# Optimization experiments

Measured on AMD Instinct MI355X. Metric: run time of the kernel, lower is better.

The kernel has to match this reference:

```python
import jax, jax.numpy as jnp
import numpy as np
import math

B, T, D, H, DM = 2, 2048, 1024, 16, 256
DK = D // H

def setup_inputs() -> dict:
    key = jax.random.key(0)
    ks = jax.random.split(key, 13)
    s = 0.02
    return {
        "Hx": jax.random.normal(ks[0], (B, D, T, 1), jnp.float32),
        "Hf": jax.random.normal(ks[1], (B, T, D), jnp.float32),
        "Gm": jax.random.normal(ks[2], (B, T, DM), jnp.float32),
        "Wg": jax.random.normal(ks[3], (T, DM), jnp.float32) * s,
        "bg": jax.random.normal(ks[4], (T,), jnp.float32) * s,
        "Wq": jax.random.normal(ks[5], (D, 2 * D), jnp.float32) * s,
        "bq": jax.random.normal(ks[6], (D,), jnp.float32) * s,
        "Wk": jax.random.normal(ks[7], (D, 2 * D), jnp.float32) * s,
        "bk": jax.random.normal(ks[8], (D,), jnp.float32) * s,
        "Wv": jax.random.normal(ks[9], (D, D), jnp.float32) * s,
        "bv": jax.random.normal(ks[10], (D,), jnp.float32) * s,
        "Wo": jax.random.normal(ks[11], (D, D), jnp.float32) * s,
        "bo": jax.random.normal(ks[12], (D,), jnp.float32) * s,
    }

def reference(Hx, Hf, Gm, Wg, bg, Wq, bq, Wk, bk, Wv, bv, Wo, bo):
    # Hx: (B, D, T, 1) -> (B, T, D)
    hx = jnp.transpose(Hx[..., 0], (0, 2, 1))
    h_cat = jnp.concatenate([hx, Hf], axis=-1)          # (B, T, 2D)
    Q = h_cat @ Wq.T + bq                               # (B, T, D)
    K = h_cat @ Wk.T + bk
    V = hx @ Wv.T + bv
    # split heads: (B, H, T, DK)
    Q = Q.reshape(B, T, H, DK).transpose(0, 2, 1, 3)
    K = K.reshape(B, T, H, DK).transpose(0, 2, 1, 3)
    V = V.reshape(B, T, H, DK).transpose(0, 2, 1, 3)
    scores = jnp.einsum('bhqd,bhkd->bhqk', Q, K) / math.sqrt(DK)
    bias = Gm @ Wg.T + bg                                # (B, T, T)
    scores = scores + bias[:, None, :, :]
    attn = jax.nn.softmax(scores, axis=-1)
    out = jnp.einsum('bhqk,bhkd->bhqd', attn, V)
    out = out.transpose(0, 2, 1, 3).reshape(B, T, D)
    return out @ Wo.T + bo
```

## Files before the change

### kernel.cpp

```cpp
#include <hip/hip_runtime.h>
#include <hip/hip_bf16.h>

using bf16 = __hip_bfloat16;
typedef __attribute__((ext_vector_type(8))) __bf16 bf16x8;
typedef __attribute__((ext_vector_type(4))) float f32x4;

#define GLB_AS(p) ((const __attribute__((address_space(1))) unsigned int*)(p))
#define LDS_AS(p) ((__attribute__((address_space(3))) unsigned int*)(p))

__device__ __forceinline__ void async_copy16(const void* g, void* l) {
  __builtin_amdgcn_global_load_lds(GLB_AS(g), LDS_AS(l), 16, 0, 0);
}

__device__ __forceinline__ f32x4 mfma16x16x32(bf16x8 a, bf16x8 b, f32x4 c) {
  return __builtin_amdgcn_mfma_f32_16x16x32_bf16(a, b, c, 0, 0, 0);
}

__device__ __forceinline__ float bfu2f(unsigned short u) {
  union { unsigned int i; float f; } x;
  x.i = (unsigned int)u << 16;
  return x.f;
}

#define LOG2E 1.44269504f

__global__ __launch_bounds__(256) void pack_hx(const float* __restrict__ Hx,
                                               bf16* __restrict__ hcat) {
  __shared__ float tile[64][65];
  const int t0 = blockIdx.x * 64, d0 = blockIdx.y * 64, b = blockIdx.z;
  const int c = threadIdx.x & 63, r0 = threadIdx.x >> 6;
#pragma unroll
  for (int i = 0; i < 16; ++i) {
    const int rd = r0 + i * 4;
    tile[rd][c] = Hx[((size_t)(b * 1024 + d0 + rd)) * 2048 + t0 + c];
  }
  __syncthreads();
#pragma unroll
  for (int i = 0; i < 16; ++i) {
    const int ct = r0 + i * 4;
    hcat[((size_t)(b * 2048 + t0 + ct)) * 2048 + d0 + c] =
        __float2bfloat16(tile[c][ct]);
  }
}

__global__ __launch_bounds__(256) void pack_all(
    const float* __restrict__ Hf, const float* __restrict__ Wq,
    const float* __restrict__ Wk, const float* __restrict__ Wv,
    const float* __restrict__ Wo, const float* __restrict__ Wg,
    const float* __restrict__ Gm, const float* __restrict__ bq,
    const float* __restrict__ bk, const float* __restrict__ bv,
    bf16* __restrict__ hcat, bf16* __restrict__ Wqkvb, bf16* __restrict__ Wob,
    bf16* __restrict__ Wgb, bf16* __restrict__ Gmb,
    float* __restrict__ qkvbias) {
  const int gid = blockIdx.x * 256 + threadIdx.x;
  const float* src = nullptr;
  bf16* dst = nullptr;
  int lg = 0, ldo = 0, off = 0, idx = 0;
  bool zero = false;
  if (gid < 1048576) { idx = gid; src = Hf; dst = hcat; lg = 8; ldo = 2048; off = 1024; }
  else if (gid < 1572864) { idx = gid - 1048576; src = Wq; dst = Wqkvb; lg = 9; ldo = 2048; }
  else if (gid < 2097152) { idx = gid - 1572864; src = Wk; dst = Wqkvb + (size_t)1024 * 2048; lg = 9; ldo = 2048; }
  else if (gid < 2359296) { idx = gid - 2097152; src = Wv; dst = Wqkvb + (size_t)2048 * 2048; lg = 8; ldo = 2048; }
  else if (gid < 2621440) { idx = gid - 2359296; zero = true; dst = Wqkvb + (size_t)2048 * 2048 + 1024; lg = 8; ldo = 2048; }
  else if (gid < 2883584) { idx = gid - 2621440; src = Wo; dst = Wob; lg = 8; ldo = 1024; }
  else if (gid < 3014656) { idx = gid - 2883584; src = Wg; dst = Wgb; lg = 6; ldo = 256; }
  else if (gid < 3276800) { idx = gid - 3014656; src = Gm; dst = Gmb; lg = 6; ldo = 256; }
  else if (gid < 3277056) { const int i = gid - 3276800; ((float4*)qkvbias)[i] = ((const float4*)bq)[i]; return; }
  else if (gid < 3277312) { const int i = gid - 3277056; ((float4*)(qkvbias + 1024))[i] = ((const float4*)bk)[i]; return; }
  else { const int i = gid - 3277312; ((float4*)(qkvbias + 2048))[i] = ((const float4*)bv)[i]; return; }
  const int row = idx >> lg, c = idx & ((1 << lg) - 1);
  bf16* o = dst + (size_t)row * ldo + off + c * 4;
  __align__(8) bf16 tmp[4];
  if (zero) {
    tmp[0] = tmp[1] = tmp[2] = tmp[3] = __float2bfloat16(0.f);
  } else {
    const float4 v = ((const float4*)src)[(size_t)idx];
    tmp[0] = __float2bfloat16(v.x); tmp[1] = __float2bfloat16(v.y);
    tmp[2] = __float2bfloat16(v.z); tmp[3] = __float2bfloat16(v.w);
  }
  *(ushort4*)o = *(const ushort4*)tmp;
}

__global__ __launch_bounds__(512, 2) void gemm_qkv_bias(
    const bf16* __restrict__ hcat, const bf16* __restrict__ Wqkv,
    const float* __restrict__ qkvbias, const bf16* __restrict__ Gmb,
    const bf16* __restrict__ Wgb, const float* __restrict__ bg,
    bf16* __restrict__ QKb, bf16* __restrict__ Vt, bf16* __restrict__ biasS) {
  __shared__ __align__(16) bf16 AS[2][256][64];
  __shared__ __align__(16) bf16 BS[2][256][64];
  const int lin = blockIdx.x;
  const bool isqkv = lin < 192;
  int m0, n0, Kd, KT, nit2;
  const bf16 *Ag, *Bg;
  const float* biasv;
  if (isqkv) {
    const int xcd = lin & 7, kk = lin >> 3;
    const int mloc = kk / 6, nloc = kk - mloc * 6;
    m0 = ((xcd >> 1) * 4 + mloc) * 256;
    n0 = ((xcd & 1) * 6 + nloc) * 256;
    Ag = hcat; Bg = Wqkv; biasv = qkvbias;
    Kd = 2048; KT = 32; nit2 = 16;
  } else {
    const int l2 = lin - 192;
    m0 = (l2 >> 3) * 256;
    n0 = (l2 & 7) * 256;
    Ag = Gmb; Bg = Wgb; biasv = bg;
    Kd = 256; KT = 4; nit2 = 2;
  }
  const int tid = threadIdx.x, lane = tid & 63, w = tid >> 6;
  const int w8 = w * 8, ln3 = lane >> 3, ch = lane & 7;
  const int fr = lane & 15, ck = lane >> 4;
  const int wm64 = (w >> 2) * 64;
  const int wn32 = (w & 3) * 32;

  f32x4 acc[8][4];
  const f32x4 fzero = {0.f, 0.f, 0.f, 0.f};
#pragma unroll
  for (int i = 0; i < 8; ++i)
#pragma unroll
    for (int j = 0; j < 4; ++j) acc[i][j] = fzero;

  auto stageA = [&](int buf, int mh, int kt) {
    const int k0 = kt * 64;
#pragma unroll
    for (int l = 0; l < 2; ++l) {
      const int rit = mh * 128 + l * 64 + w8 + ln3;
      async_copy16(Ag + (size_t)(m0 + rit) * Kd + k0 + ((ch ^ ln3) << 3),
                   (char*)&AS[buf][0][0] + ((mh * 128 + l * 64 + w8) << 7));
    }
  };
  auto stageB = [&](int buf, int nh, int kt) {
    const int k0 = kt * 64;
#pragma unroll
    for (int l = 0; l < 2; ++l) {
      const int rit = nh * 128 + l * 64 + w8 + ln3;
      async_copy16(Bg + (size_t)(n0 + rit) * Kd + k0 + ((ch ^ ln3) << 3),
                   (char*)&BS[buf][0][0] + ((nh * 128 + l * 64 + w8) << 7));
    }
  };

  bf16x8 af[4][2], bA[2][2], bB[2][2];
  auto ldA = [&](int buf, int mh) {
#pragma unroll
    for (int i = 0; i < 4; ++i)
#pragma unroll
      for (int ks = 0; ks < 2; ++ks)
        af[i][ks] = *(const bf16x8*)(
            &AS[buf][mh * 128 + wm64 + i * 16 + fr][0] +
            (((ks * 4 + ck) ^ (fr & 7)) << 3));
  };
  auto ldB = [&](bf16x8 (&dst)[2][2], int buf, int nh) {
#pragma unroll
    for (int j = 0; j < 2; ++j)
#pragma unroll
      for (int ks = 0; ks < 2; ++ks)
        dst[j][ks] = *(const bf16x8*)(
            &BS[buf][nh * 128 + wn32 + j * 16 + fr][0] +
            (((ks * 4 + ck) ^ (fr & 7)) << 3));
  };

#define BAR() __builtin_amdgcn_s_barrier()
#define LGKM0() asm volatile("s_waitcnt lgkmcnt(0)" ::: "memory")
#define MMAQ(MH, NH, BF)                                                      \
  __builtin_amdgcn_s_setprio(1);                                              \
  _Pragma("unroll") for (int i_ = 0; i_ < 4; ++i_) {                          \
    _Pragma("unroll") for (int j_ = 0; j_ < 2; ++j_) {                        \
      acc[(MH) * 4 + i_][(NH) * 2 + j_] = mfma16x16x32(                       \
          af[i_][0], BF[j_][0], acc[(MH) * 4 + i_][(NH) * 2 + j_]);           \
      acc[(MH) * 4 + i_][(NH) * 2 + j_] = mfma16x16x32(                       \
          af[i_][1], BF[j_][1], acc[(MH) * 4 + i_][(NH) * 2 + j_]);           \
    }                                                                         \
  }                                                                           \
  __builtin_amdgcn_s_setprio(0);

  stageA(0, 0, 0); stageB(0, 0, 0); stageB(0, 1, 0); stageA(0, 1, 0);
  stageA(1, 0, 1); stageB(1, 0, 1);
  asm volatile("s_waitcnt vmcnt(4)" ::: "memory");
  BAR();

  for (int it = 0; it < nit2; ++it) {
    const int kodd = 2 * it + 1;
    const int kn0 = (2 * it + 2 < KT) ? 2 * it + 2 : KT - 1;
    const int kn1 = (2 * it + 3 < KT) ? 2 * it + 3 : KT - 1;

    ldA(0, 0); ldB(bA, 0, 0);
    stageB(1, 1, kodd);
    asm volatile("s_waitcnt lgkmcnt(8)");
    BAR(); LGKM0();
    MMAQ(0, 0, bA);
    BAR();
    ldB(bB, 0, 1);
    stageA(1, 1, kodd);
    BAR(); LGKM0();
    MMAQ(0, 1, bB);
    BAR();
    ldA(0, 1);
    stageA(0, 0, kn0);
    BAR(); LGKM0();
    MMAQ(1, 0, bA);
    BAR();
    stageB(0, 0, kn0);
    asm volatile("s_waitcnt vmcnt(4)" ::: "memory");
    BAR();
    MMAQ(1, 1, bB);
    BAR();
    ldA(1, 0); ldB(bA, 1, 0);
    stageB(0, 1, kn0);
    asm volatile("s_waitcnt lgkmcnt(8)");
    BAR(); LGKM0();
    MMAQ(0, 0, bA);
    BAR();
    ldB(bB, 1, 1);
    stageA(0, 1, kn0);
    BAR(); LGKM0();
    MMAQ(0, 1, bB);
    BAR();
    ldA(1, 1);
    stageA(1, 0, kn1);
    BAR(); LGKM0();
    MMAQ(1, 0, bA);
    BAR();
    stageB(1, 0, kn1);
    asm volatile("s_waitcnt vmcnt(4)" ::: "memory");
    BAR();
    MMAQ(1, 1, bB);
    BAR();
  }
  asm volatile("s_waitcnt vmcnt(0)" ::: "memory");

  const int erow = (lane >> 4) * 4, ecol = lane & 15;
  if (!isqkv) {
#pragma unroll
    for (int ai = 0; ai < 8; ++ai) {
      const int gm0 = m0 + (ai >> 2) * 128 + wm64 + (ai & 3) * 16 + erow;
#pragma unroll
      for (int bj = 0; bj < 4; ++bj) {
        const int gn = n0 + (bj >> 1) * 128 + wn32 + (bj & 1) * 16 + ecol;
        const float bv = biasv[gn];
#pragma unroll
        for (int r = 0; r < 4; ++r)
          biasS[(size_t)(gm0 + r) * 2048 + gn] =
              __float2bfloat16((acc[ai][bj][r] + bv) * LOG2E);
      }
    }
  } else if (n0 < 2048) {
    const float sc = (n0 < 1024) ? 0.125f * LOG2E : 1.0f;
#pragma unroll
    for (int ai = 0; ai < 8; ++ai) {
      const int gm0 = m0 + (ai >> 2) * 128 + wm64 + (ai & 3) * 16 + erow;
#pragma unroll
      for (int bj = 0; bj < 4; ++bj) {
        const int gn = n0 + (bj >> 1) * 128 + wn32 + (bj & 1) * 16 + ecol;
        const float bv = biasv[gn];
#pragma unroll
        for (int r = 0; r < 4; ++r)
          QKb[(size_t)(gm0 + r) * 2048 + gn] =
              __float2bfloat16((acc[ai][bj][r] + bv) * sc);
      }
    }
  } else {
#pragma unroll
    for (int ai = 0; ai < 8; ++ai) {
      const int gm0 = m0 + (ai >> 2) * 128 + wm64 + (ai & 3) * 16 + erow;
      const int bb = gm0 >> 11;
      const int t = gm0 & 2047;
#pragma unroll
      for (int bj = 0; bj < 4; ++bj) {
        const int gn = n0 + (bj >> 1) * 128 + wn32 + (bj & 1) * 16 + ecol;
        const float bv = biasv[gn];
        const int d = gn - 2048;
        __align__(8) bf16 tmp[4];
#pragma unroll
        for (int r = 0; r < 4; ++r)
          tmp[r] = __float2bfloat16(acc[ai][bj][r] + bv);
        *(ushort4*)(Vt + ((size_t)(bb * 1024 + d)) * 2048 + t) =
            *(const ushort4*)tmp;
      }
    }
  }
#undef MMAQ
#undef LGKM0
#undef BAR
}

__global__ __launch_bounds__(256) void gemm_out(const bf16* __restrict__ A,
                                                const bf16* __restrict__ W,
                                                const float* __restrict__ biasv,
                                                float* __restrict__ C) {
  __shared__ __align__(16) bf16 As[2][128 * 64];
  __shared__ __align__(16) bf16 Bs[2][64 * 64];
  const int lin = blockIdx.x;
  const int xcd = lin & 7;
  const int kk = lin >> 3;
  const int m0 = (kk >> 1) * 128;
  const int n0 = (xcd * 2 + (kk & 1)) * 64;
  const int tid = threadIdx.x, lane = tid & 63, w = tid >> 6;
  const int wm = (w >> 1) * 64, wn = (w & 1) * 32;
  const int fr = lane & 15;
  const int ck = lane >> 4;

  f32x4 acc[4][2];
  const f32x4 fzero = {0.f, 0.f, 0.f, 0.f};
#pragma unroll
  for (int i = 0; i < 4; ++i)
#pragma unroll
    for (int j = 0; j < 2; ++j) acc[i][j] = fzero;

  auto stage = [&](int it, int buf) {
    const int k0 = it * 64;
#pragma unroll
    for (int is = 0; is < 4; ++is) {
      const int off = is * 4096 + w * 1024;
      const int row = (off >> 7) + (lane >> 3);
      const int sch = ((lane & 7) ^ (row & 7)) * 8;
      async_copy16(A + (size_t)(m0 + row) * 1024 + k0 + sch,
                   (char*)As[buf] + off);
      if (is < 2)
        async_copy16(W + (size_t)(n0 + row) * 1024 + k0 + sch,
                     (char*)Bs[buf] + off);
    }
  };

  stage(0, 0);
  __syncthreads();
  for (int it = 0; it < 16; ++it) {
    const int cur = it & 1;
    if (it + 1 < 16) stage(it + 1, cur ^ 1);
#pragma unroll
    for (int ks = 0; ks < 2; ++ks) {
      bf16x8 af[4], bfr[2];
      const int swk0 = (((ks * 4 + ck) ^ (fr & 7))) * 8;
#pragma unroll
      for (int i = 0; i < 4; ++i)
        af[i] = *(const bf16x8*)(As[cur] + (wm + i * 16 + fr) * 64 + swk0);
#pragma unroll
      for (int j = 0; j < 2; ++j)
        bfr[j] = *(const bf16x8*)(Bs[cur] + (wn + j * 16 + fr) * 64 + swk0);
#pragma unroll
      for (int i = 0; i < 4; ++i)
#pragma unroll
        for (int j = 0; j < 2; ++j)
          acc[i][j] = mfma16x16x32(af[i], bfr[j], acc[i][j]);
    }
    __syncthreads();
  }
  const int erow = (lane >> 4) * 4;
  const int ecol = lane & 15;
#pragma unroll
  for (int i = 0; i < 4; ++i) {
    const int gm0 = m0 + wm + i * 16 + erow;
#pragma unroll
    for (int j = 0; j < 2; ++j) {
      const int gn = n0 + wn + j * 16 + ecol;
      const float bv = biasv[gn];
#pragma unroll
      for (int r = 0; r < 4; ++r)
        C[(size_t)(gm0 + r) * 1024 + gn] = acc[i][j][r] + bv;
    }
  }
}

__global__ __launch_bounds__(512, 2) void flash_attn(
    const bf16* __restrict__ Qm, const bf16* __restrict__ Km,
    const bf16* __restrict__ Vtm, const bf16* __restrict__ biasS,
    float* __restrict__ Op0, float* __restrict__ Op1,
    float* __restrict__ lpart) {
  __shared__ __align__(16) bf16 Ks[2][2][64 * 64];
  __shared__ __align__(16) bf16 Vs[2][2][64 * 64];
  __shared__ __align__(16) bf16 Ps[8 * 32 * 72];
  const int lin = blockIdx.x;
  const int hp = lin >> 5;
  const int g = lin & 31;
  const int half = g & 1;
  const int b = (g >> 1) & 1;
  const int q0 = (g >> 2) * 256;
  const int tid = threadIdx.x, lane = tid & 63, w = tid >> 6;
  const int ql = lane & 15, qk = lane >> 4;
  const int T = 2048, D = 1024;
  const int sw0 = (qk ^ (ql & 7)) * 8;
  const int sw1 = ((qk + 4) ^ (ql & 7)) * 8;
  const int ln3 = lane >> 3;
  const int sch = ((lane & 7) ^ ln3) << 3;
  const int jb = half * 16;

  bf16x8 qf[2][2][2];
#pragma unroll
  for (int hh = 0; hh < 2; ++hh)
#pragma unroll
    for (int qt = 0; qt < 2; ++qt)
#pragma unroll
      for (int ks = 0; ks < 2; ++ks)
        qf[hh][qt][ks] = *(const bf16x8*)(
            Qm + (size_t)(b * T + q0 + w * 32 + qt * 16 + ql) * 2048 +
            (hp * 2 + hh) * 64 + ks * 32 + qk * 8);

  f32x4 acc[2][4][2];
  const f32x4 fzero = {0.f, 0.f, 0.f, 0.f};
#pragma unroll
  for (int hh = 0; hh < 2; ++hh)
#pragma unroll
    for (int dt = 0; dt < 4; ++dt)
#pragma unroll
      for (int qt = 0; qt < 2; ++qt) acc[hh][dt][qt] = fzero;
  float lp[2][2] = {{0.f, 0.f}, {0.f, 0.f}};

  const bf16* kbase0 = Km + (size_t)(b * T) * 2048 + (hp * 2) * 64;
  const bf16* vbase0 = Vtm + (size_t)(b * D + hp * 2 * 64) * 2048;
  const bf16* bb0 = biasS + (size_t)(b * T + q0 + w * 32 + ql) * 2048 + qk * 4;
  bf16* pb = Ps + w * 2304;
  const int srow = w * 8 + ln3;

  ushort4 bqA[2][4], bqB[2][4];

#define STAGEKV(BUF, JJ)                                                       \
  _Pragma("unroll") for (int hh_ = 0; hh_ < 2; ++hh_) {                        \
    async_copy16(kbase0 + (size_t)((JJ) * 64 + srow) * 2048 + hh_ * 64 + sch,  \
                 (char*)Ks[BUF][hh_] + w * 1024);                              \
    async_copy16(vbase0 + (size_t)(hh_ * 64 + srow) * 2048 + (JJ) * 64 + sch,  \
                 (char*)Vs[BUF][hh_] + w * 1024);                              \
  }

  STAGEKV(0, jb)
#pragma unroll
  for (int qt = 0; qt < 2; ++qt)
#pragma unroll
    for (int jt = 0; jt < 4; ++jt)
      bqA[qt][jt] =
          *(const ushort4*)(bb0 + (size_t)qt * 16 * 2048 + jb * 64 + jt * 16);

#define QKHEAD(HH, CUR, BQC)                                                   \
  {                                                                            \
    const bf16* ksp_ = Ks[CUR][HH];                                            \
    _Pragma("unroll") for (int jt_ = 0; jt_ < 4; ++jt_) {                      \
      const bf16x8 kf0_ = *(const bf16x8*)(ksp_ + (jt_ * 16 + ql) * 64 + sw0); \
      const bf16x8 kf1_ = *(const bf16x8*)(ksp_ + (jt_ * 16 + ql) * 64 + sw1); \
      _Pragma("unroll") for (int qt_ = 0; qt_ < 2; ++qt_) {                    \
        f32x4 c_;                                                              \
        c_[0] = bfu2f(BQC[qt_][jt_].x); c_[1] = bfu2f(BQC[qt_][jt_].y);        \
        c_[2] = bfu2f(BQC[qt_][jt_].z); c_[3] = bfu2f(BQC[qt_][jt_].w);        \
        c_ = mfma16x16x32(kf0_, qf[HH][qt_][0], c_);                           \
        c_ = mfma16x16x32(kf1_, qf[HH][qt_][1], c_);                           \
        __align__(8) bf16 t4_[4];                                              \
        _Pragma("unroll") for (int r_ = 0; r_ < 4; ++r_) {                     \
          const float pv_ = __builtin_amdgcn_exp2f(c_[r_]);                    \
          lp[HH][qt_] += pv_;                                                  \
          t4_[r_] = __float2bfloat16(pv_);                                     \
        }                                                                      \
        *(ushort4*)(pb + (qt_ * 16 + ql) * 72 + jt_ * 16 + qk * 4) =           \
            *(const ushort4*)t4_;                                              \
      }                                                                        \
    }                                                                          \
  }

#define PVHEAD(HH, CUR)                                                        \
  {                                                                            \
    const bf16* vsp_ = Vs[CUR][HH];                                            \
    __builtin_amdgcn_s_setprio(1);                                             \
    _Pragma("unroll") for (int ks_ = 0; ks_ < 2; ++ks_) {                      \
      const bf16x8 pf0_ = *(const bf16x8*)(pb + ql * 72 + ks_ * 32 + qk * 8);  \
      const bf16x8 pf1_ =                                                      \
          *(const bf16x8*)(pb + (16 + ql) * 72 + ks_ * 32 + qk * 8);           \
      const int sw_ = ks_ ? sw1 : sw0;                                         \
      _Pragma("unroll") for (int dt_ = 0; dt_ < 4; ++dt_) {                    \
        const bf16x8 vf_ =                                                     \
            *(const bf16x8*)(vsp_ + (dt_ * 16 + ql) * 64 + sw_);               \
        acc[HH][dt_][0] = mfma16x16x32(pf0_, vf_, acc[HH][dt_][0]);            \
        acc[HH][dt_][1] = mfma16x16x32(pf1_, vf_, acc[HH][dt_][1]);            \
      }                                                                        \
    }                                                                          \
    __builtin_amdgcn_s_setprio(0);                                             \
  }

#define AITER(JV, CUR, BQC, BQN)                                               \
  {                                                                            \
    const int jn_ = (JV) < 15 ? (JV) + 1 : 15;                                 \
    const int jjn_ = jb + jn_;                                                 \
    STAGEKV((CUR) ^ 1, jjn_)                                                   \
    _Pragma("unroll") for (int qt_ = 0; qt_ < 2; ++qt_)                        \
        _Pragma("unroll") for (int jt_ = 0; jt_ < 4; ++jt_)                    \
            BQN[qt_][jt_] = *(const ushort4*)(bb0 + (size_t)qt_ * 16 * 2048 +  \
                                              jjn_ * 64 + jt_ * 16);           \
    asm volatile("s_waitcnt vmcnt(12)" ::: "memory");                          \
    __builtin_amdgcn_s_barrier();                                              \
    QKHEAD(0, CUR, BQC)                                                        \
    PVHEAD(0, CUR)                                                             \
    QKHEAD(1, CUR, BQC)                                                        \
    PVHEAD(1, CUR)                                                             \
    __builtin_amdgcn_s_barrier();                                              \
  }

  for (int jp = 0; jp < 8; ++jp) {
    AITER(jp * 2, 0, bqA, bqB)
    AITER(jp * 2 + 1, 1, bqB, bqA)
  }
#undef AITER
#undef QKHEAD
#undef PVHEAD
#undef STAGEKV
  asm volatile("s_waitcnt vmcnt(0)" ::: "memory");

#pragma unroll
  for (int hh = 0; hh < 2; ++hh)
#pragma unroll
    for (int qt = 0; qt < 2; ++qt) {
      lp[hh][qt] += __shfl_xor(lp[hh][qt], 16);
      lp[hh][qt] += __shfl_xor(lp[hh][qt], 32);
    }
  if (qk == 0) {
#pragma unroll
    for (int hh = 0; hh < 2; ++hh)
#pragma unroll
      for (int qt = 0; qt < 2; ++qt)
        lpart[half * 65536 + (b * 16 + hp * 2 + hh) * 2048 + q0 + w * 32 +
              qt * 16 + ql] = lp[hh][qt];
  }
  float* Op = half ? Op1 : Op0;
#pragma unroll
  for (int hh = 0; hh < 2; ++hh)
#pragma unroll
    for (int qt = 0; qt < 2; ++qt)
#pragma unroll
      for (int r = 0; r < 4; ++r) {
        const size_t orow =
            (size_t)(b * T + q0 + w * 32 + qt * 16 + qk * 4 + r);
#pragma unroll
        for (int dt = 0; dt < 4; ++dt)
          Op[orow * 1024 + (hp * 2 + hh) * 64 + dt * 16 + ql] =
              acc[hh][dt][qt][r];
      }
}

__global__ __launch_bounds__(256) void combine(const float* __restrict__ O0,
                                               const float* __restrict__ O1,
                                               const float* __restrict__ lpart,
                                               bf16* __restrict__ AOut) {
  const int idx = blockIdx.x * 256 + threadIdx.x;
  const int row = idx >> 8;
  const int col = (idx & 255) * 4;
  const int b = row >> 11, q = row & 2047, h = col >> 6;
  const int li = (b * 16 + h) * 2048 + q;
  const float inv = __builtin_amdgcn_rcpf(lpart[li] + lpart[65536 + li]);
  const float4 a = *(const float4*)(O0 + (size_t)row * 1024 + col);
  const float4 c = *(const float4*)(O1 + (size_t)row * 1024 + col);
  __align__(8) bf16 t[4] = {
      __float2bfloat16((a.x + c.x) * inv), __float2bfloat16((a.y + c.y) * inv),
      __float2bfloat16((a.z + c.z) * inv), __float2bfloat16((a.w + c.w) * inv)};
  *(ushort4*)(AOut + (size_t)row * 1024 + col) = *(const ushort4*)t;
}

extern "C" void kernel_launch(void* const* d_in, const int* in_sizes, int n_in,
                              void* d_out, int out_size, void* d_ws,
                              size_t ws_size, hipStream_t stream) {
  (void)in_sizes; (void)n_in; (void)out_size; (void)ws_size;
  const float* Hx = (const float*)d_in[0];
  const float* Hf = (const float*)d_in[1];
  const float* Gm = (const float*)d_in[2];
  const float* Wg = (const float*)d_in[3];
  const float* bg = (const float*)d_in[4];
  const float* Wq = (const float*)d_in[5];
  const float* bq = (const float*)d_in[6];
  const float* Wk = (const float*)d_in[7];
  const float* bk = (const float*)d_in[8];
  const float* Wv = (const float*)d_in[9];
  const float* bv = (const float*)d_in[10];
  const float* Wo = (const float*)d_in[11];
  const float* bo = (const float*)d_in[12];
  float* out = (float*)d_out;

  char* p = (char*)d_ws;
  bf16* hcat = (bf16*)p;   p += (size_t)4096 * 2048 * 2;
  bf16* QKb = (bf16*)p;    p += (size_t)4096 * 2048 * 2;
  bf16* Vtb = (bf16*)p;    p += (size_t)4096 * 1024 * 2;
  bf16* biasS = (bf16*)p;  p += (size_t)4096 * 2048 * 2;
  bf16* AOut = (bf16*)p;   p += (size_t)4096 * 1024 * 2;
  bf16* Wqkvb = (bf16*)p;  p += (size_t)3072 * 2048 * 2;
  bf16* Wob = (bf16*)p;    p += (size_t)1024 * 1024 * 2;
  bf16* Wgb = (bf16*)p;    p += (size_t)2048 * 256 * 2;
  bf16* Gmb = (bf16*)p;    p += (size_t)4096 * 256 * 2;
  float* qkvbias = (float*)p; p += (size_t)3072 * 4;
  float* Op1 = (float*)p;  p += (size_t)4096 * 1024 * 4;
  float* lpart = (float*)p; p += (size_t)2 * 65536 * 4;
  float* Op0 = (float*)hcat;

  pack_hx<<<dim3(32, 16, 2), 256, 0, stream>>>(Hx, hcat);
  pack_all<<<dim3(12803), 256, 0, stream>>>(Hf, Wq, Wk, Wv, Wo, Wg, Gm, bq, bk,
                                            bv, hcat, Wqkvb, Wob, Wgb, Gmb,
                                            qkvbias);
  gemm_qkv_bias<<<dim3(320), 512, 0, stream>>>(hcat, Wqkvb, qkvbias, Gmb,
                                               Wgb, bg, QKb, Vtb, biasS);
  flash_attn<<<dim3(256), 512, 0, stream>>>(QKb, QKb + 1024, Vtb, biasS,
                                            Op0, Op1, lpart);
  combine<<<dim3(4096), 256, 0, stream>>>(Op0, Op1, lpart, AOut);
  gemm_out<<<dim3(512), 256, 0, stream>>>(AOut, Wob, bo, out);
}
```

Before: 280.3 us.

## Split flash attention to one head per block with swizzled unpadded P tile

Each flash_attn block now handles one head instead of a pair, which doubles the grid to 512 blocks and halves the LDS and register footprint so launch bounds can request four blocks per CU. The padded P buffer is replaced by a 64-wide XOR-swizzled layout to avoid bank conflicts without padding. The block-index decode is reordered and the vmcnt wait is adjusted for fewer outstanding copies. In exchange, the bias tile is now read separately for each head, doubling bias traffic, and the work done between barriers is halved.

```diff
diff --git a/kernel.cpp b/kernel.cpp
--- a/kernel.cpp
+++ b/kernel.cpp
@@ -360,20 +360,21 @@
   }
 }
 
-__global__ __launch_bounds__(512, 2) void flash_attn(
+__global__ __launch_bounds__(512, 4) void flash_attn(
     const bf16* __restrict__ Qm, const bf16* __restrict__ Km,
     const bf16* __restrict__ Vtm, const bf16* __restrict__ biasS,
     float* __restrict__ Op0, float* __restrict__ Op1,
     float* __restrict__ lpart) {
-  __shared__ __align__(16) bf16 Ks[2][2][64 * 64];
-  __shared__ __align__(16) bf16 Vs[2][2][64 * 64];
-  __shared__ __align__(16) bf16 Ps[8 * 32 * 72];
+  __shared__ __align__(16) bf16 Ks[2][64 * 64];
+  __shared__ __align__(16) bf16 Vs[2][64 * 64];
+  __shared__ __align__(16) bf16 Ps[8 * 32 * 64];
   const int lin = blockIdx.x;
-  const int hp = lin >> 5;
+  const int h = lin >> 5;
   const int g = lin & 31;
-  const int half = g & 1;
-  const int b = (g >> 1) & 1;
-  const int q0 = (g >> 2) * 256;
+  const int qblk = g >> 2;
+  const int half = (g >> 1) & 1;
+  const int b = g & 1;
+  const int q0 = qblk * 256;
   const int tid = threadIdx.x, lane = tid & 63, w = tid >> 6;
   const int ql = lane & 15, qk = lane >> 4;
   const int T = 2048, D = 1024;
@@ -382,42 +383,39 @@
   const int ln3 = lane >> 3;
   const int sch = ((lane & 7) ^ ln3) << 3;
   const int jb = half * 16;
-
-  bf16x8 qf[2][2][2];
-#pragma unroll
-  for (int hh = 0; hh < 2; ++hh)
-#pragma unroll
-    for (int qt = 0; qt < 2; ++qt)
-#pragma unroll
-      for (int ks = 0; ks < 2; ++ks)
-        qf[hh][qt][ks] = *(const bf16x8*)(
-            Qm + (size_t)(b * T + q0 + w * 32 + qt * 16 + ql) * 2048 +
-            (hp * 2 + hh) * 64 + ks * 32 + qk * 8);
-
-  f32x4 acc[2][4][2];
+  const int qla7 = ql & 7;
+
+  bf16x8 qf[2][2];
+#pragma unroll
+  for (int qt = 0; qt < 2; ++qt)
+#pragma unroll
+    for (int ks = 0; ks < 2; ++ks)
+      qf[qt][ks] = *(const bf16x8*)(
+          Qm + (size_t)(b * T + q0 + w * 32 + qt * 16 + ql) * 2048 + h * 64 +
+          ks * 32 + qk * 8);
+
+  f32x4 acc[4][2];
   const f32x4 fzero = {0.f, 0.f, 0.f, 0.f};
 #pragma unroll
-  for (int hh = 0; hh < 2; ++hh)
-#pragma unroll
-    for (int dt = 0; dt < 4; ++dt)
-#pragma unroll
-      for (int qt = 0; qt < 2; ++qt) acc[hh][dt][qt] = fzero;
-  float lp[2][2] = {{0.f, 0.f}, {0.f, 0.f}};
-
-  const bf16* kbase0 = Km + (size_t)(b * T) * 2048 + (hp * 2) * 64;
-  const bf16* vbase0 = Vtm + (size_t)(b * D + hp * 2 * 64) * 2048;
+  for (int dt = 0; dt < 4; ++dt)
+#pragma unroll
+    for (int qt = 0; qt < 2; ++qt) acc[dt][qt] = fzero;
+  float lp[2] = {0.f, 0.f};
+
+  const bf16* kbase = Km + (size_t)(b * T) * 2048 + h * 64;
+  const bf16* vbase = Vtm + (size_t)(b * D + h * 64) * 2048;
   const bf16* bb0 = biasS + (size_t)(b * T + q0 + w * 32 + ql) * 2048 + qk * 4;
-  bf16* pb = Ps + w * 2304;
+  bf16* pb = Ps + w * 2048;
   const int srow = w * 8 + ln3;
 
   ushort4 bqA[2][4], bqB[2][4];
 
 #define STAGEKV(BUF, JJ)                                                       \
-  _Pragma("unroll") for (int hh_ = 0; hh_ < 2; ++hh_) {                        \
-    async_copy16(kbase0 + (size_t)((JJ) * 64 + srow) * 2048 + hh_ * 64 + sch,  \
-                 (char*)Ks[BUF][hh_] + w * 1024);                              \
-    async_copy16(vbase0 + (size_t)(hh_ * 64 + srow) * 2048 + (JJ) * 64 + sch,  \
-                 (char*)Vs[BUF][hh_] + w * 1024);                              \
+  {                                                                            \
+    async_copy16(kbase + (size_t)((JJ) * 64 + srow) * 2048 + sch,              \
+                 (char*)Ks[BUF] + w * 1024);                                   \
+    async_copy16(vbase + (size_t)srow * 2048 + (JJ) * 64 + sch,                \
+                 (char*)Vs[BUF] + w * 1024);                                   \
   }
 
   STAGEKV(0, jb)
@@ -428,44 +426,44 @@
       bqA[qt][jt] =
           *(const ushort4*)(bb0 + (size_t)qt * 16 * 2048 + jb * 64 + jt * 16);
 
-#define QKHEAD(HH, CUR, BQC)                                                   \
+#define QKHEAD(CUR, BQC)                                                       \
   {                                                                            \
-    const bf16* ksp_ = Ks[CUR][HH];                                            \
+    const bf16* ksp_ = Ks[CUR];                                                \
     _Pragma("unroll") for (int jt_ = 0; jt_ < 4; ++jt_) {                      \
       const bf16x8 kf0_ = *(const bf16x8*)(ksp_ + (jt_ * 16 + ql) * 64 + sw0); \
       const bf16x8 kf1_ = *(const bf16x8*)(ksp_ + (jt_ * 16 + ql) * 64 + sw1); \
+      const int pch_ = (((jt_ * 2 + (qk >> 1)) ^ qla7) << 3) + ((qk & 1) << 2);\
       _Pragma("unroll") for (int qt_ = 0; qt_ < 2; ++qt_) {                    \
         f32x4 c_;                                                              \
         c_[0] = bfu2f(BQC[qt_][jt_].x); c_[1] = bfu2f(BQC[qt_][jt_].y);        \
         c_[2] = bfu2f(BQC[qt_][jt_].z); c_[3] = bfu2f(BQC[qt_][jt_].w);        \
-        c_ = mfma16x16x32(kf0_, qf[HH][qt_][0], c_);                           \
-        c_ = mfma16x16x32(kf1_, qf[HH][qt_][1], c_);                           \
+        c_ = mfma16x16x32(kf0_, qf[qt_][0], c_);                               \
+        c_ = mfma16x16x32(kf1_, qf[qt_][1], c_);                               \
         __align__(8) bf16 t4_[4];                                              \
         _Pragma("unroll") for (int r_ = 0; r_ < 4; ++r_) {                     \
           const float pv_ = __builtin_amdgcn_exp2f(c_[r_]);                    \
-          lp[HH][qt_] += pv_;                                                  \
+          lp[qt_] += pv_;                                                      \
           t4_[r_] = __float2bfloat16(pv_);                                     \
         }                                                                      \
-        *(ushort4*)(pb + (qt_ * 16 + ql) * 72 + jt_ * 16 + qk * 4) =           \
-            *(const ushort4*)t4_;                                              \
+        *(ushort4*)(pb + (qt_ * 16 + ql) * 64 + pch_) = *(const ushort4*)t4_;  \
       }                                                                        \
     }                                                                          \
   }
 
-#define PVHEAD(HH, CUR)                                                        \
+#define PVHEAD(CUR)                                                            \
   {                                                                            \
-    const bf16* vsp_ = Vs[CUR][HH];                                            \
+    const bf16* vsp_ = Vs[CUR];                                                \
     __builtin_amdgcn_s_setprio(1);                                             \
     _Pragma("unroll") for (int ks_ = 0; ks_ < 2; ++ks_) {                      \
-      const bf16x8 pf0_ = *(const bf16x8*)(pb + ql * 72 + ks_ * 32 + qk * 8);  \
-      const bf16x8 pf1_ =                                                      \
-          *(const bf16x8*)(pb + (16 + ql) * 72 + ks_ * 32 + qk * 8);           \
+      const int psw_ = (((ks_ * 4 + qk) ^ qla7) << 3);                         \
+      const bf16x8 pf0_ = *(const bf16x8*)(pb + ql * 64 + psw_);               \
+      const bf16x8 pf1_ = *(const bf16x8*)(pb + (16 + ql) * 64 + psw_);        \
       const int sw_ = ks_ ? sw1 : sw0;                                         \
       _Pragma("unroll") for (int dt_ = 0; dt_ < 4; ++dt_) {                    \
         const bf16x8 vf_ =                                                     \
             *(const bf16x8*)(vsp_ + (dt_ * 16 + ql) * 64 + sw_);               \
-        acc[HH][dt_][0] = mfma16x16x32(pf0_, vf_, acc[HH][dt_][0]);            \
-        acc[HH][dt_][1] = mfma16x16x32(pf1_, vf_, acc[HH][dt_][1]);            \
+        acc[dt_][0] = mfma16x16x32(pf0_, vf_, acc[dt_][0]);                    \
+        acc[dt_][1] = mfma16x16x32(pf1_, vf_, acc[dt_][1]);                    \
       }                                                                        \
     }                                                                          \
     __builtin_amdgcn_s_setprio(0);                                             \
@@ -480,12 +478,10 @@
         _Pragma("unroll") for (int jt_ = 0; jt_ < 4; ++jt_)                    \
             BQN[qt_][jt_] = *(const ushort4*)(bb0 + (size_t)qt_ * 16 * 2048 +  \
                                               jjn_ * 64 + jt_ * 16);           \
-    asm volatile("s_waitcnt vmcnt(12)" ::: "memory");                          \
+    asm volatile("s_waitcnt vmcnt(10)" ::: "memory");                          \
     __builtin_amdgcn_s_barrier();                                              \
-    QKHEAD(0, CUR, BQC)                                                        \
-    PVHEAD(0, CUR)                                                             \
-    QKHEAD(1, CUR, BQC)                                                        \
-    PVHEAD(1, CUR)                                                             \
+    QKHEAD(CUR, BQC)                                                           \
+    PVHEAD(CUR)                                                                \
     __builtin_amdgcn_s_barrier();                                              \
   }
 
@@ -500,34 +496,26 @@
   asm volatile("s_waitcnt vmcnt(0)" ::: "memory");
 
 #pragma unroll
-  for (int hh = 0; hh < 2; ++hh)
-#pragma unroll
-    for (int qt = 0; qt < 2; ++qt) {
-      lp[hh][qt] += __shfl_xor(lp[hh][qt], 16);
-      lp[hh][qt] += __shfl_xor(lp[hh][qt], 32);
-    }
+  for (int qt = 0; qt < 2; ++qt) {
+    lp[qt] += __shfl_xor(lp[qt], 16);
+    lp[qt] += __shfl_xor(lp[qt], 32);
+  }
   if (qk == 0) {
 #pragma unroll
-    for (int hh = 0; hh < 2; ++hh)
-#pragma unroll
-      for (int qt = 0; qt < 2; ++qt)
-        lpart[half * 65536 + (b * 16 + hp * 2 + hh) * 2048 + q0 + w * 32 +
-              qt * 16 + ql] = lp[hh][qt];
+    for (int qt = 0; qt < 2; ++qt)
+      lpart[half * 65536 + (b * 16 + h) * 2048 + q0 + w * 32 + qt * 16 + ql] =
+          lp[qt];
   }
   float* Op = half ? Op1 : Op0;
 #pragma unroll
-  for (int hh = 0; hh < 2; ++hh)
-#pragma unroll
-    for (int qt = 0; qt < 2; ++qt)
-#pragma unroll
-      for (int r = 0; r < 4; ++r) {
-        const size_t orow =
-            (size_t)(b * T + q0 + w * 32 + qt * 16 + qk * 4 + r);
-#pragma unroll
-        for (int dt = 0; dt < 4; ++dt)
-          Op[orow * 1024 + (hp * 2 + hh) * 64 + dt * 16 + ql] =
-              acc[hh][dt][qt][r];
-      }
+  for (int qt = 0; qt < 2; ++qt)
+#pragma unroll
+    for (int r = 0; r < 4; ++r) {
+      const size_t orow = (size_t)(b * T + q0 + w * 32 + qt * 16 + qk * 4 + r);
+#pragma unroll
+      for (int dt = 0; dt < 4; ++dt)
+        Op[orow * 1024 + h * 64 + dt * 16 + ql] = acc[dt][qt][r];
+    }
 }
 
 __global__ __launch_bounds__(256) void combine(const float* __restrict__ O0,
@@ -588,7 +576,7 @@
                                             qkvbias);
   gemm_qkv_bias<<<dim3(320), 512, 0, stream>>>(hcat, Wqkvb, qkvbias, Gmb,
                                                Wgb, bg, QKb, Vtb, biasS);
-  flash_attn<<<dim3(256), 512, 0, stream>>>(QKb, QKb + 1024, Vtb, biasS,
+  flash_attn<<<dim3(512), 512, 0, stream>>>(QKb, QKb + 1024, Vtb, biasS,
                                             Op0, Op1, lpart);
   combine<<<dim3(4096), 256, 0, stream>>>(Op0, Op1, lpart, AOut);
   gemm_out<<<dim3(512), 256, 0, stream>>>(AOut, Wob, bo, out);
```

After: 295.3 us. +5.4%, slower.
